# Performance work log

Hardware: AMD Instinct MI355X
Metric: run time of the kernel (lower is better)

The kernel has to match this reference:

```python
import jax, jax.numpy as jnp
import numpy as np
import math

D_MODEL = 1024
D_HEAD = 64
N_HEADS = D_MODEL // D_HEAD  # 16
COND = 768
EPS = 1e-6


def make_freqs():
    # AxialRoPE(dim=d_head//2, n_heads): freqs linspace in log-space, reshaped [dim//4, nh].T
    dim = D_HEAD // 2  # 32
    n = N_HEADS * dim // 4  # 128
    log_min = math.log(math.pi)
    log_max = math.log(10.0 * math.pi)
    freqs = jnp.exp(jnp.linspace(log_min, log_max, n + 1, dtype=jnp.float32)[:-1])
    return freqs.reshape(dim // 4, N_HEADS).T  # [n_heads, d_head//8] = [16, 8]


def setup_inputs() -> dict:
    key = jax.random.key(0)
    ks = jax.random.split(key, 6)
    N, H, W = 8, 32, 32
    x = jax.random.normal(ks[0], (N, H, W, D_MODEL), jnp.float32)
    pos = jax.random.uniform(ks[1], (N, H, W, 2), jnp.float32) * 2.0 - 1.0
    cond = jax.random.normal(ks[2], (N, COND), jnp.float32)
    norm_w = jax.random.normal(ks[3], (D_MODEL, COND), jnp.float32) * 0.02
    qkv_w = jax.random.normal(ks[4], (3 * D_MODEL, D_MODEL), jnp.float32) / math.sqrt(D_MODEL)
    out_w = jax.random.normal(ks[5], (D_MODEL, D_MODEL), jnp.float32) * 0.02
    scale = jnp.full((N_HEADS,), 10.0, jnp.float32)
    return {"x": x, "pos": pos, "cond": cond, "norm_w": norm_w,
            "qkv_w": qkv_w, "out_w": out_w, "scale": scale}


def rms_norm(x, scale, eps):
    mean_sq = jnp.mean(x * x, axis=-1, keepdims=True)
    return x * (scale * jax.lax.rsqrt(mean_sq + eps))


def apply_rotary(x, theta):
    # rotate first 2*d dims of the head; rest passes through
    d = theta.shape[-1]
    x1, x2, rest = x[..., :d], x[..., d:2 * d], x[..., 2 * d:]
    cos, sin = jnp.cos(theta), jnp.sin(theta)
    return jnp.concatenate([x1 * cos - x2 * sin, x2 * cos + x1 * sin, rest], axis=-1)


def reference(x, pos, cond, norm_w, qkv_w, out_w, scale):
    N, H, W, _ = x.shape
    S = H * W
    skip = x
    # AdaRMSNorm: scale = zero-init linear(cond) + 1
    ns = cond @ norm_w.T  # [N, d_model]
    xn = rms_norm(x, ns[:, None, None, :] + 1.0, EPS)
    # QKV projection, split 'n h w (t nh e)'
    qkv = (xn @ qkv_w.T).reshape(N, S, 3, N_HEADS, D_HEAD)
    q = jnp.transpose(qkv[:, :, 0], (0, 2, 1, 3))  # [N, nh, S, e]
    k = jnp.transpose(qkv[:, :, 1], (0, 2, 1, 3))
    v = jnp.transpose(qkv[:, :, 2], (0, 2, 1, 3))
    # cosine-sim scaling: per-head learned scale, L2-normalize q,k
    sqrt_scale = jnp.sqrt(scale)[:, None, None]  # [nh,1,1]
    q = q * (sqrt_scale * jax.lax.rsqrt(jnp.sum(q * q, -1, keepdims=True) + EPS))
    k = k * (sqrt_scale * jax.lax.rsqrt(jnp.sum(k * k, -1, keepdims=True) + EPS))
    # axial RoPE theta
    freqs = make_freqs()  # [nh, d_head//8]
    pos_f = pos.reshape(N, S, 2)
    theta_h = pos_f[:, :, None, 0:1] * freqs  # [N,S,nh,8]
    theta_w = pos_f[:, :, None, 1:2] * freqs
    theta = jnp.concatenate([theta_h, theta_w], axis=-1)  # [N,S,nh,16]
    theta = jnp.transpose(theta, (0, 2, 1, 3))  # [N,nh,S,16]
    q = apply_rotary(q, theta)
    k = apply_rotary(k, theta)
    # attention with scale=1.0 (cosine-sim already scaled)
    scores = jnp.einsum('bhqe,bhke->bhqk', q, k)
    probs = jax.nn.softmax(scores, axis=-1)
    o = jnp.einsum('bhqk,bhke->bhqe', probs, v)  # [N,nh,S,e]
    o = jnp.transpose(o, (0, 2, 1, 3)).reshape(N, H, W, D_MODEL)
    return o @ out_w.T + skip
```

## Files before the change

kernel.cpp:

```cpp
#include <hip/hip_runtime.h>
#include <hip/hip_bf16.h>
#include <math.h>

typedef __bf16 bf16;
typedef __bf16 bf16x8 __attribute__((ext_vector_type(8)));
typedef __bf16 bf16x4 __attribute__((ext_vector_type(4)));
typedef float f32x4 __attribute__((ext_vector_type(4)));

#define MFMA16(a, b, c) __builtin_amdgcn_mfma_f32_16x16x32_bf16((a), (b), (c), 0, 0, 0)

__device__ __forceinline__ void gload_lds16(const void* g, void* l) {
  __builtin_amdgcn_global_load_lds((__attribute__((address_space(1))) void*)(g),
                                   (__attribute__((address_space(3))) void*)(l),
                                   16, 0, 0);
}

__global__ __launch_bounds__(256) void f2bf_kernel(const float* __restrict__ in,
                                                   bf16* __restrict__ out, int n4) {
  int i = blockIdx.x * 256 + threadIdx.x;
  if (i >= n4) return;
  float4 v = ((const float4*)in)[i];
  bf16x4 o;
  o[0] = (bf16)v.x; o[1] = (bf16)v.y; o[2] = (bf16)v.z; o[3] = (bf16)v.w;
  *(bf16x4*)(out + (size_t)i * 4) = o;
}

__global__ __launch_bounds__(256) void ns_kernel(const float* __restrict__ cond,
                                                 const float* __restrict__ norm_w,
                                                 float* __restrict__ nsp1) {
  int tid = blockIdx.x * 256 + threadIdx.x;
  int b = tid >> 10, c = tid & 1023;
  const float4* wv = (const float4*)(norm_w + (size_t)c * 768);
  const float4* cv = (const float4*)(cond + (size_t)b * 768);
  float acc = 0.f;
#pragma unroll 8
  for (int i = 0; i < 192; ++i) {
    float4 w4 = wv[i], c4 = cv[i];
    acc += w4.x * c4.x + w4.y * c4.y + w4.z * c4.z + w4.w * c4.w;
  }
  nsp1[tid] = acc + 1.0f;
}

__global__ __launch_bounds__(256) void rmsnorm_kernel(const float* __restrict__ x,
                                                      const float* __restrict__ nsp1,
                                                      bf16* __restrict__ xn) {
  int lane = threadIdx.x & 63, w = threadIdx.x >> 6;
  int m = blockIdx.x * 4 + w;
  int b = m >> 10;
  const float* xp = x + (size_t)m * 1024 + lane * 16;
  float v[16];
  float ss = 0.f;
#pragma unroll
  for (int i = 0; i < 4; ++i) {
    float4 t4 = ((const float4*)xp)[i];
    v[4 * i + 0] = t4.x; v[4 * i + 1] = t4.y; v[4 * i + 2] = t4.z; v[4 * i + 3] = t4.w;
    ss += t4.x * t4.x + t4.y * t4.y + t4.z * t4.z + t4.w * t4.w;
  }
#pragma unroll
  for (int off = 32; off >= 1; off >>= 1) ss += __shfl_xor(ss, off);
  float r = rsqrtf(ss * (1.0f / 1024.0f) + 1e-6f);
  const float* np = nsp1 + (size_t)b * 1024 + lane * 16;
  bf16x8 o0, o1;
#pragma unroll
  for (int j = 0; j < 8; ++j) o0[j] = (bf16)(v[j] * np[j] * r);
#pragma unroll
  for (int j = 0; j < 8; ++j) o1[j] = (bf16)(v[8 + j] * np[8 + j] * r);
  bf16* op = xn + (size_t)m * 1024 + lane * 16;
  *(bf16x8*)op = o0;
  *(bf16x8*)(op + 8) = o1;
}

template <int MODE>
__global__ __launch_bounds__(512, 2) void gemm256b(const bf16* __restrict__ A,
                                                   const bf16* __restrict__ B, int nbn,
                                                   bf16* __restrict__ qout, bf16* __restrict__ kout,
                                                   bf16* __restrict__ vtout, float* __restrict__ fout,
                                                   const float* __restrict__ skip,
                                                   const float* __restrict__ pos,
                                                   const float* __restrict__ scale) {
  constexpr int K = 1024;
  __shared__ __align__(16) bf16 sm[24576];
  const int t = threadIdx.x;
  const int cpx = gridDim.x >> 3;
  const int bid = blockIdx.x;
  const int virt = (bid & 7) * cpx + (bid >> 3);
  const int bn = virt % nbn, bm = virt / nbn;
  const int m0 = bm * 256, n0 = bn * 128;
  const int lane = t & 63, wid = t >> 6;
  const int wr = wid >> 1, wc = wid & 1;
  const int r16 = lane & 15, hi = lane >> 4;

  const int tq = t >> 3, c8 = t & 7, cp = c8 ^ (tq & 7);
  const size_t gA = (size_t)(m0 + tq * 2 + (cp >> 2)) * K + (cp & 3) * 8;
  const size_t gB = (size_t)(n0 + tq * 2 + (cp >> 2)) * K + (cp & 3) * 8;
  const size_t gj = (size_t)128 * K;
  const int ldst = t * 8;

  const int chunk = ((r16 & 1) * 4 + hi) ^ (r16 >> 1);
  int aoff[4], boff[4];
#pragma unroll
  for (int fr = 0; fr < 4; ++fr) aoff[fr] = (wr * 32 + fr * 8 + (r16 >> 1)) * 64 + chunk * 8;
#pragma unroll
  for (int fc = 0; fc < 4; ++fc)
    boff[fc] = (wc * 32 + fc * 8 + (r16 >> 1)) * 64 + chunk * 8 + 8192;

  f32x4 acc[4][4] = {};
  constexpr int NS = K >> 5;

#define STG(tile, slot)                                              \
  {                                                                  \
    const bf16* as_ = A + gA + (size_t)(tile) * 32;                  \
    const bf16* bs_ = B + gB + (size_t)(tile) * 32;                  \
    gload_lds16(as_, &sm[(slot) * 12288 + ldst]);                    \
    gload_lds16(as_ + gj, &sm[(slot) * 12288 + 4096 + ldst]);        \
    gload_lds16(bs_, &sm[(slot) * 12288 + 8192 + ldst]);             \
  }

  STG(0, 0);
  STG(1, 1);

  for (int s = 0; s < NS; ++s) {
    if (s < NS - 1) {
      asm volatile("s_waitcnt vmcnt(3)" ::: "memory");
    } else {
      asm volatile("s_waitcnt vmcnt(0)" ::: "memory");
    }
    __builtin_amdgcn_s_barrier();
    __builtin_amdgcn_sched_barrier(0);
    bf16x8 af[4], bfr[4];
    const bf16* base = &sm[(s & 1) * 12288];
#pragma unroll
    for (int fr = 0; fr < 4; ++fr) af[fr] = *(const bf16x8*)&base[aoff[fr]];
#pragma unroll
    for (int fc = 0; fc < 4; ++fc) bfr[fc] = *(const bf16x8*)&base[boff[fc]];
    asm volatile("s_waitcnt lgkmcnt(0)" ::: "memory");
    __builtin_amdgcn_sched_barrier(0);
    __builtin_amdgcn_s_barrier();
    __builtin_amdgcn_sched_barrier(0);
    if (s + 2 < NS) STG(s + 2, s & 1);
    __builtin_amdgcn_s_setprio(1);
#pragma unroll
    for (int fc = 0; fc < 4; ++fc)
#pragma unroll
      for (int fr = 0; fr < 4; ++fr) acc[fr][fc] = MFMA16(af[fr], bfr[fc], acc[fr][fc]);
    __builtin_amdgcn_s_setprio(0);
  }
#undef STG

  if constexpr (MODE == 0) {
    const int p = n0 >> 10;
    if (p == 2) {
#pragma unroll
      for (int fr = 0; fr < 4; ++fr) {
        int mrow = m0 + wr * 64 + fr * 16 + hi * 4;
        int b = mrow >> 10, s0 = mrow & 1023;
#pragma unroll
        for (int fc = 0; fc < 4; ++fc) {
          int n = n0 + wc * 64 + fc * 16 + r16;
          int d = n & 63, hh = (n >> 6) & 15;
          bf16x4 pk;
          pk[0] = (bf16)acc[fr][fc][0]; pk[1] = (bf16)acc[fr][fc][1];
          pk[2] = (bf16)acc[fr][fc][2]; pk[3] = (bf16)acc[fr][fc][3];
          *(bf16x4*)&vtout[(((size_t)(b * 16 + hh) * 64 + d) << 10) + s0] = pk;
        }
      }
    } else {
      const int hh = ((n0 + wc * 64) >> 6) & 15;
      const float LOG2E = 1.4426950408889634f;
      const float sqv = sqrtf(scale[hh]) * (p == 0 ? LOG2E : 1.0f);
      const float f = __expf(1.14472988584940017f +
                             0.0179897502011134460f * (float)((r16 & 7) * 16 + hh));
      const bool is_h = (r16 < 8);
      bf16* dst = (p == 0) ? qout : kout;
#pragma unroll
      for (int fr = 0; fr < 4; ++fr) {
        int mrow = m0 + wr * 64 + fr * 16 + hi * 4;
        int b = mrow >> 10, s0 = mrow & 1023;
        float rr[4];
#pragma unroll
        for (int r = 0; r < 4; ++r) {
          float ss = acc[fr][0][r] * acc[fr][0][r] + acc[fr][1][r] * acc[fr][1][r] +
                     acc[fr][2][r] * acc[fr][2][r] + acc[fr][3][r] * acc[fr][3][r];
          ss += __shfl_xor(ss, 1);
          ss += __shfl_xor(ss, 2);
          ss += __shfl_xor(ss, 4);
          ss += __shfl_xor(ss, 8);
          rr[r] = sqv * rsqrtf(ss + 1e-6f);
        }
#pragma unroll
        for (int r = 0; r < 4; ++r) {
          float2 pp = *(const float2*)&pos[(((size_t)b << 10) + s0 + r) * 2];
          float th = (is_h ? pp.x : pp.y) * f;
          float sv, cv;
          __sincosf(th, &sv, &cv);
          float x1 = acc[fr][0][r] * rr[r];
          float x2 = acc[fr][1][r] * rr[r];
          size_t rowb = (((size_t)(b * 16 + hh) << 10) + s0 + r) * 64;
          dst[rowb + r16]      = (bf16)(x1 * cv - x2 * sv);
          dst[rowb + 16 + r16] = (bf16)(x2 * cv + x1 * sv);
          dst[rowb + 32 + r16] = (bf16)(acc[fr][2][r] * rr[r]);
          dst[rowb + 48 + r16] = (bf16)(acc[fr][3][r] * rr[r]);
        }
      }
    }
  } else {
#pragma unroll
    for (int fr = 0; fr < 4; ++fr) {
      int mrow = m0 + wr * 64 + fr * 16 + hi * 4;
#pragma unroll
      for (int fc = 0; fc < 4; ++fc) {
        int n = n0 + wc * 64 + fc * 16 + r16;
#pragma unroll
        for (int r = 0; r < 4; ++r) {
          size_t off = (size_t)(mrow + r) * 1024 + n;
          fout[off] = acc[fr][fc][r] + skip[off];
        }
      }
    }
  }
}

__global__ __launch_bounds__(256, 4) void attn_kernel(const bf16* __restrict__ q,
                                                      const bf16* __restrict__ k,
                                                      const bf16* __restrict__ vt,
                                                      bf16* __restrict__ o) {
  int bid = blockIdx.x;
  int virt = (bid & 7) * 256 + (bid >> 3);
  const int bh = virt >> 4;
  const int qt = virt & 15;
  const int b = bh >> 4, h = bh & 15;
  const int t = threadIdx.x, lane = t & 63, w = t >> 6;
  const int r16 = lane & 15, hi = lane >> 4;
  const int swp = r16 & 7;

  __shared__ bf16 lK[2][4096];
  __shared__ bf16 lV[2][4096];
  __shared__ bf16 lP[4][1024];
  bf16* myp = lP[w];

  const bf16* kp = k + (size_t)bh * 65536;
  const bf16* vp = vt + (size_t)bh * 65536;

  const bf16* qp = q + ((size_t)bh * 1024 + qt * 64 + w * 16) * 64;
  bf16x8 aq0 = *(const bf16x8*)&qp[r16 * 64 + hi * 8];
  bf16x8 aq1 = *(const bf16x8*)&qp[r16 * 64 + 32 + hi * 8];

  bf16x8 ones;
#pragma unroll
  for (int i = 0; i < 8; ++i) ones[i] = (bf16)1.0f;

  const int srow0 = t >> 3, sc0 = t & 7;

  f32x4 oacc[4] = {};
  f32x4 lacc = {};

#pragma unroll
  for (int j = 0; j < 2; ++j) {
    int row = srow0 + j * 32;
    int se = ((sc0 ^ (row & 7)) << 3);
    gload_lds16(kp + (size_t)row * 64 + se, &lK[0][t * 8 + j * 2048]);
    gload_lds16(vp + (size_t)row * 1024 + se, &lV[0][t * 8 + j * 2048]);
  }
  __syncthreads();

  int cur = 0;
  for (int kt = 0; kt < 16; ++kt) {
    if (kt < 15) {
      const bf16* kt_base = kp + (kt + 1) * 4096;
      const bf16* vt_base = vp + (kt + 1) * 64;
#pragma unroll
      for (int j = 0; j < 2; ++j) {
        int row = srow0 + j * 32;
        int se = ((sc0 ^ (row & 7)) << 3);
        gload_lds16(kt_base + (size_t)row * 64 + se, &lK[cur ^ 1][t * 8 + j * 2048]);
        gload_lds16(vt_base + (size_t)row * 1024 + se, &lV[cur ^ 1][t * 8 + j * 2048]);
      }
    }
    f32x4 sT[4] = {};
    __builtin_amdgcn_s_setprio(1);
#pragma unroll
    for (int c = 0; c < 4; ++c) {
      int row = c * 16 + r16, sw = row & 7;
      bf16x8 bk0 = *(const bf16x8*)&lK[cur][row * 64 + ((hi ^ sw) << 3)];
      bf16x8 bk1 = *(const bf16x8*)&lK[cur][row * 64 + (((hi + 4) ^ sw) << 3)];
      sT[c] = MFMA16(bk0, aq0, sT[c]);
      sT[c] = MFMA16(bk1, aq1, sT[c]);
    }
    __builtin_amdgcn_s_setprio(0);
    bf16x4 pb[4];
#pragma unroll
    for (int c = 0; c < 4; ++c) {
#pragma unroll
      for (int r = 0; r < 4; ++r) pb[c][r] = (bf16)exp2f(sT[c][r]);
    }
#pragma unroll
    for (int c = 0; c < 4; ++c) {
      int eoff = r16 * 64 + (((c * 32 + hi * 8) ^ (swp << 4)) >> 1);
      *(bf16x4*)&myp[eoff] = pb[c];
    }
    {
      bf16x8 pa0 = *(const bf16x8*)&myp[r16 * 64 + ((hi ^ swp) << 3)];
      bf16x8 pa1 = *(const bf16x8*)&myp[r16 * 64 + (((hi + 4) ^ swp) << 3)];
      __builtin_amdgcn_s_setprio(1);
#pragma unroll
      for (int c = 0; c < 4; ++c) {
        int row = c * 16 + r16, sw = row & 7;
        bf16x8 bv0 = *(const bf16x8*)&lV[cur][row * 64 + ((hi ^ sw) << 3)];
        bf16x8 bv1 = *(const bf16x8*)&lV[cur][row * 64 + (((hi + 4) ^ sw) << 3)];
        oacc[c] = MFMA16(pa0, bv0, oacc[c]);
        oacc[c] = MFMA16(pa1, bv1, oacc[c]);
      }
      lacc = MFMA16(pa0, ones, lacc);
      lacc = MFMA16(pa1, ones, lacc);
      __builtin_amdgcn_s_setprio(0);
    }
    __syncthreads();
    cur ^= 1;
  }
  f32x4 inv;
#pragma unroll
  for (int r = 0; r < 4; ++r) inv[r] = 1.f / lacc[r];
#pragma unroll
  for (int c = 0; c < 4; ++c) {
#pragma unroll
    for (int r = 0; r < 4; ++r) {
      int srow = qt * 64 + w * 16 + hi * 4 + r;
      o[((size_t)b * 1024 + srow) * 1024 + h * 64 + c * 16 + r16] =
          (bf16)(oacc[c][r] * inv[r]);
    }
  }
}

extern "C" void kernel_launch(void* const* d_in, const int* in_sizes, int n_in,
                              void* d_out, int out_size, void* d_ws, size_t ws_size,
                              hipStream_t stream) {
  const float* x      = (const float*)d_in[0];
  const float* pos    = (const float*)d_in[1];
  const float* cond   = (const float*)d_in[2];
  const float* norm_w = (const float*)d_in[3];
  const float* qkv_w  = (const float*)d_in[4];
  const float* out_w  = (const float*)d_in[5];
  const float* scale  = (const float*)d_in[6];
  float* out = (float*)d_out;

  char* ws = (char*)d_ws;
  bf16* xn        = (bf16*)(ws + 0);
  bf16* qkv_w_bf  = (bf16*)(ws + 16777216);
  bf16* out_w_bf  = (bf16*)(ws + 23068672);
  float* nsp1     = (float*)(ws + 25165824);
  bf16* qraw      = (bf16*)(ws + 25198592);
  bf16* kraw      = (bf16*)(ws + 41975808);
  bf16* vt        = (bf16*)(ws + 58753024);
  bf16* o_attn    = xn;

  f2bf_kernel<<<3072, 256, 0, stream>>>(qkv_w, qkv_w_bf, 786432);
  f2bf_kernel<<<1024, 256, 0, stream>>>(out_w, out_w_bf, 262144);
  ns_kernel<<<32, 256, 0, stream>>>(cond, norm_w, nsp1);
  rmsnorm_kernel<<<2048, 256, 0, stream>>>(x, nsp1, xn);
  gemm256b<0><<<768, 512, 0, stream>>>(xn, qkv_w_bf, 24, qraw, kraw, vt, nullptr, nullptr,
                                       pos, scale);
  attn_kernel<<<2048, 256, 0, stream>>>(qraw, kraw, vt, o_attn);
  gemm256b<1><<<256, 512, 0, stream>>>(o_attn, out_w_bf, 8, nullptr, nullptr, nullptr, out, x,
                                       nullptr, nullptr);
}
```

Before: 198.8 us.

## Switch attention to 32x32 MFMA tiles and keep probabilities in registers

The attention kernel now uses 32x32x16 bf16 MFMA with 32 query rows per wave and 128 per block, so half as many blocks are launched. The scores are computed transposed so the exp'd probability fragments can feed the PV MFMA straight from registers, which removes the LDS round-trip through the lP buffer. Each K/V tile loaded into LDS is reused across twice as many queries. In exchange the accumulators need more registers (launch bounds occupancy hint lowered from 4 to 3), and the V fragments are now gathered with two 4-element LDS reads per MFMA.

```diff
diff --git a/kernel.cpp b/kernel.cpp
--- a/kernel.cpp
+++ b/kernel.cpp
@@ -6,8 +6,10 @@
 typedef __bf16 bf16x8 __attribute__((ext_vector_type(8)));
 typedef __bf16 bf16x4 __attribute__((ext_vector_type(4)));
 typedef float f32x4 __attribute__((ext_vector_type(4)));
+typedef float f32x16 __attribute__((ext_vector_type(16)));
 
 #define MFMA16(a, b, c) __builtin_amdgcn_mfma_f32_16x16x32_bf16((a), (b), (c), 0, 0, 0)
+#define MFMA32(a, b, c) __builtin_amdgcn_mfma_f32_32x32x16_bf16((a), (b), (c), 0, 0, 0)
 
 __device__ __forceinline__ void gload_lds16(const void* g, void* l) {
   __builtin_amdgcn_global_load_lds((__attribute__((address_space(1))) void*)(g),
@@ -220,30 +222,29 @@
   }
 }
 
-__global__ __launch_bounds__(256, 4) void attn_kernel(const bf16* __restrict__ q,
+__global__ __launch_bounds__(256, 3) void attn_kernel(const bf16* __restrict__ q,
                                                       const bf16* __restrict__ k,
                                                       const bf16* __restrict__ vt,
                                                       bf16* __restrict__ o) {
   int bid = blockIdx.x;
-  int virt = (bid & 7) * 256 + (bid >> 3);
-  const int bh = virt >> 4;
-  const int qt = virt & 15;
+  int virt = (bid & 7) * 128 + (bid >> 3);
+  const int bh = virt >> 3;
+  const int qt = virt & 7;
   const int b = bh >> 4, h = bh & 15;
   const int t = threadIdx.x, lane = t & 63, w = t >> 6;
-  const int r16 = lane & 15, hi = lane >> 4;
-  const int swp = r16 & 7;
+  const int l31 = lane & 31, h2 = lane >> 5;
 
   __shared__ bf16 lK[2][4096];
   __shared__ bf16 lV[2][4096];
-  __shared__ bf16 lP[4][1024];
-  bf16* myp = lP[w];
 
   const bf16* kp = k + (size_t)bh * 65536;
   const bf16* vp = vt + (size_t)bh * 65536;
 
-  const bf16* qp = q + ((size_t)bh * 1024 + qt * 64 + w * 16) * 64;
-  bf16x8 aq0 = *(const bf16x8*)&qp[r16 * 64 + hi * 8];
-  bf16x8 aq1 = *(const bf16x8*)&qp[r16 * 64 + 32 + hi * 8];
+  const bf16* qp = q + ((size_t)bh * 1024 + qt * 128 + w * 32) * 64;
+  bf16x8 qf[4];
+#pragma unroll
+  for (int df = 0; df < 4; ++df)
+    qf[df] = *(const bf16x8*)&qp[l31 * 64 + df * 16 + h2 * 8];
 
   bf16x8 ones;
 #pragma unroll
@@ -251,8 +252,7 @@
 
   const int srow0 = t >> 3, sc0 = t & 7;
 
-  f32x4 oacc[4] = {};
-  f32x4 lacc = {};
+  f32x16 oacc0 = {}, oacc1 = {}, lacc = {};
 
 #pragma unroll
   for (int j = 0; j < 2; ++j) {
@@ -276,58 +276,56 @@
         gload_lds16(vt_base + (size_t)row * 1024 + se, &lV[cur ^ 1][t * 8 + j * 2048]);
       }
     }
-    f32x4 sT[4] = {};
+    f32x16 sa0 = {}, sa1 = {};
     __builtin_amdgcn_s_setprio(1);
 #pragma unroll
-    for (int c = 0; c < 4; ++c) {
-      int row = c * 16 + r16, sw = row & 7;
-      bf16x8 bk0 = *(const bf16x8*)&lK[cur][row * 64 + ((hi ^ sw) << 3)];
-      bf16x8 bk1 = *(const bf16x8*)&lK[cur][row * 64 + (((hi + 4) ^ sw) << 3)];
-      sT[c] = MFMA16(bk0, aq0, sT[c]);
-      sT[c] = MFMA16(bk1, aq1, sT[c]);
+    for (int df = 0; df < 4; ++df) {
+      int sw = l31 & 7;
+      int ce = (((2 * df + h2) ^ sw) << 3);
+      bf16x8 kf0 = *(const bf16x8*)&lK[cur][l31 * 64 + ce];
+      bf16x8 kf1 = *(const bf16x8*)&lK[cur][(32 + l31) * 64 + ce];
+      sa0 = MFMA32(kf0, qf[df], sa0);
+      sa1 = MFMA32(kf1, qf[df], sa1);
     }
     __builtin_amdgcn_s_setprio(0);
-    bf16x4 pb[4];
-#pragma unroll
-    for (int c = 0; c < 4; ++c) {
-#pragma unroll
-      for (int r = 0; r < 4; ++r) pb[c][r] = (bf16)exp2f(sT[c][r]);
-    }
-#pragma unroll
-    for (int c = 0; c < 4; ++c) {
-      int eoff = r16 * 64 + (((c * 32 + hi * 8) ^ (swp << 4)) >> 1);
-      *(bf16x4*)&myp[eoff] = pb[c];
-    }
-    {
-      bf16x8 pa0 = *(const bf16x8*)&myp[r16 * 64 + ((hi ^ swp) << 3)];
-      bf16x8 pa1 = *(const bf16x8*)&myp[r16 * 64 + (((hi + 4) ^ swp) << 3)];
-      __builtin_amdgcn_s_setprio(1);
-#pragma unroll
-      for (int c = 0; c < 4; ++c) {
-        int row = c * 16 + r16, sw = row & 7;
-        bf16x8 bv0 = *(const bf16x8*)&lV[cur][row * 64 + ((hi ^ sw) << 3)];
-        bf16x8 bv1 = *(const bf16x8*)&lV[cur][row * 64 + (((hi + 4) ^ sw) << 3)];
-        oacc[c] = MFMA16(pa0, bv0, oacc[c]);
-        oacc[c] = MFMA16(pa1, bv1, oacc[c]);
-      }
-      lacc = MFMA16(pa0, ones, lacc);
-      lacc = MFMA16(pa1, ones, lacc);
-      __builtin_amdgcn_s_setprio(0);
-    }
+    bf16x8 pa[4];
+#pragma unroll
+    for (int e = 0; e < 8; ++e) {
+      pa[0][e] = (bf16)exp2f(sa0[e]);
+      pa[1][e] = (bf16)exp2f(sa0[e + 8]);
+      pa[2][e] = (bf16)exp2f(sa1[e]);
+      pa[3][e] = (bf16)exp2f(sa1[e + 8]);
+    }
+    __builtin_amdgcn_s_setprio(1);
+#pragma unroll
+    for (int pk = 0; pk < 4; ++pk) {
+      lacc = MFMA32(pa[pk], ones, lacc);
+#pragma unroll
+      for (int db = 0; db < 2; ++db) {
+        int row = db * 32 + l31, sw = row & 7;
+        const bf16* vb = &lV[cur][row * 64];
+        bf16x4 v0 = *(const bf16x4*)&vb[(((2 * pk) ^ sw) << 3) + 4 * h2];
+        bf16x4 v1 = *(const bf16x4*)&vb[(((2 * pk + 1) ^ sw) << 3) + 4 * h2];
+        bf16x8 vf;
+        vf[0] = v0[0]; vf[1] = v0[1]; vf[2] = v0[2]; vf[3] = v0[3];
+        vf[4] = v1[0]; vf[5] = v1[1]; vf[6] = v1[2]; vf[7] = v1[3];
+        if (db == 0) oacc0 = MFMA32(pa[pk], vf, oacc0);
+        else         oacc1 = MFMA32(pa[pk], vf, oacc1);
+      }
+    }
+    __builtin_amdgcn_s_setprio(0);
     __syncthreads();
     cur ^= 1;
   }
-  f32x4 inv;
-#pragma unroll
-  for (int r = 0; r < 4; ++r) inv[r] = 1.f / lacc[r];
-#pragma unroll
-  for (int c = 0; c < 4; ++c) {
-#pragma unroll
-    for (int r = 0; r < 4; ++r) {
-      int srow = qt * 64 + w * 16 + hi * 4 + r;
-      o[((size_t)b * 1024 + srow) * 1024 + h * 64 + c * 16 + r16] =
-          (bf16)(oacc[c][r] * inv[r]);
-    }
+  f32x16 inv;
+#pragma unroll
+  for (int r = 0; r < 16; ++r) inv[r] = 1.f / lacc[r];
+#pragma unroll
+  for (int r = 0; r < 16; ++r) {
+    int qrow = qt * 128 + w * 32 + (r & 3) + 8 * (r >> 2) + 4 * h2;
+    size_t rowb = ((size_t)b * 1024 + qrow) * 1024 + h * 64;
+    o[rowb + l31]      = (bf16)(oacc0[r] * inv[r]);
+    o[rowb + 32 + l31] = (bf16)(oacc1[r] * inv[r]);
   }
 }
 
@@ -359,7 +357,7 @@
   rmsnorm_kernel<<<2048, 256, 0, stream>>>(x, nsp1, xn);
   gemm256b<0><<<768, 512, 0, stream>>>(xn, qkv_w_bf, 24, qraw, kraw, vt, nullptr, nullptr,
                                        pos, scale);
-  attn_kernel<<<2048, 256, 0, stream>>>(qraw, kraw, vt, o_attn);
+  attn_kernel<<<1024, 256, 0, stream>>>(qraw, kraw, vt, o_attn);
   gemm256b<1><<<256, 512, 0, stream>>>(o_attn, out_w_bf, 8, nullptr, nullptr, nullptr, out, x,
                                        nullptr, nullptr);
 }
```

Measured after the change: 199.0 us. Within noise of the previous version (+0.1%).
